# Kernel optimization log

Measured on AMD Instinct MI355X. Metric: run time of the kernel, lower is better.

Reference implementation:

```python
import jax, jax.numpy as jnp
import numpy as np

ALPHA, BETA, THRESH, T = 0.9, 0.8, 1.0, 10


def _heaviside(x):
    return (x > 0).astype(x.dtype)


def _conv(x, w, b, stride):
    y = jax.lax.conv_general_dilated(
        x, w, window_strides=(stride, stride), padding='VALID',
        dimension_numbers=('NCHW', 'OIHW', 'NCHW'))
    return jax.nn.relu(y + b[None, :, None, None])


def setup_inputs() -> dict:
    key = jax.random.key(0)
    ks = jax.random.split(key, 16)
    B = 128
    state = jax.random.uniform(ks[0], (B, 3, 224, 224), dtype=jnp.float32)
    history = jax.random.uniform(ks[1], (B, 90), dtype=jnp.float32)
    fc_in = 64 * 24 * 24 + 90  # 36954

    def w(k, shape, fan_in):
        return jax.random.normal(k, shape, dtype=jnp.float32) * (1.0 / np.sqrt(fan_in))

    return {
        'state': state, 'history': history,
        'cw1': w(ks[2], (32, 3, 8, 8), 3 * 8 * 8), 'cb1': jnp.zeros((32,), jnp.float32),
        'cw2': w(ks[3], (64, 32, 4, 4), 32 * 4 * 4), 'cb2': jnp.zeros((64,), jnp.float32),
        'cw3': w(ks[4], (64, 64, 3, 3), 64 * 3 * 3), 'cb3': jnp.zeros((64,), jnp.float32),
        'w1': w(ks[5], (128, fc_in), fc_in), 'b1': jnp.zeros((128,), jnp.float32),
        'w2': w(ks[6], (256, 128), 128), 'b2': jnp.zeros((256,), jnp.float32),
        'w3': w(ks[7], (9, 256), 256), 'b3': jnp.zeros((9,), jnp.float32),
    }


def reference(state, history, cw1, cb1, cw2, cb2, cw3, cb3, w1, b1, w2, b2, w3, b3):
    B = state.shape[0]
    f = _conv(state, cw1, cb1, 4)
    f = _conv(f, cw2, cb2, 2)
    f = _conv(f, cw3, cb3, 1)
    x = jnp.concatenate([f.reshape(B, -1), history], axis=1)  # (B, 36954)
    # encoding='constant' -> input (hence h1) is identical every timestep
    h1 = x @ w1.T + b1  # (B,128)

    def lif(h, mem, syn):
        new_syn = ALPHA * syn + h
        new_mem = BETA * mem + new_syn
        out = _heaviside(new_mem - THRESH)
        return out, new_mem - out * THRESH, new_syn

    z = lambda d: jnp.zeros((B, d), x.dtype)
    carry0 = (z(128), z(128), z(256), z(256), z(9), z(9), z(9))

    def step(carry, _):
        mem1, syn1, mem2, syn2, mem3, syn3, pot = carry
        spk1, mem1, syn1 = lif(h1, mem1, syn1)
        h2 = spk1 @ w2.T + b2
        spk2, mem2, syn2 = lif(h2, mem2, syn2)
        h3 = spk2 @ w3.T + b3
        syn3 = ALPHA * syn3 + h3
        mem3 = BETA * mem3 + syn3
        pot = pot + mem3
        return (mem1, syn1, mem2, syn2, mem3, syn3, pot), None

    carry, _ = jax.lax.scan(step, carry0, None, length=T)
    return carry[6] / T
```

## Files before the change

kernel.cpp:

```cpp
#include <hip/hip_runtime.h>

#define ALPHA 0.9f
#define BETA  0.8f
#define XS 36960

typedef _Float16 f16;
typedef _Float16 f16x8 __attribute__((ext_vector_type(8)));
typedef float f32x4 __attribute__((ext_vector_type(4)));


__global__ __launch_bounds__(256) void prep_weights_kernel(
    const float* __restrict__ cw1, const float* __restrict__ cw2,
    const float* __restrict__ cw3, const float* __restrict__ w2,
    f16* __restrict__ w1h, f16* __restrict__ w1l,
    f16* __restrict__ w2h, f16* __restrict__ w2l,
    f16* __restrict__ w3h, f16* __restrict__ w3l,
    float* __restrict__ w2q) {
  int i = blockIdx.x * 256 + threadIdx.x;
  if (i < 6144)  { float v = cw1[i]; f16 h = (f16)v; w1h[i] = h; w1l[i] = (f16)(v - (float)h); }
  if (i < 32768) { float v = cw2[i]; f16 h = (f16)v; w2h[i] = h; w2l[i] = (f16)(v - (float)h); }
  if (i < 49152) {
    int oc = i / 768, r = i % 768;
    int c = r / 12, rr = r % 12, kh = rr >> 2, kw = rr & 3;
    float v = (kw < 3) ? cw3[oc * 576 + c * 9 + kh * 3 + kw] : 0.f;
    f16 h = (f16)v; w3h[i] = h; w3l[i] = (f16)(v - (float)h);
  }
  if (i < 32768) {
    int j = i >> 7, k = i & 127;
    w2q[((k >> 2) * 256 + j) * 4 + (k & 3)] = w2[i];
  }
}

__global__ __launch_bounds__(256) void pad_w1_kernel(
    const float* __restrict__ w1, float* __restrict__ w1p) {
  int i = blockIdx.x * 256 + threadIdx.x;
  if (i < 128 * 18480) {
    int j = i / 18480, c = i - j * 18480;
    float2 v;
    if (c < 18477) v = *(const float2*)&w1[(size_t)j * 36954 + c * 2];
    else v = make_float2(0.f, 0.f);
    *(float2*)&w1p[(size_t)j * XS + c * 2] = v;
  }
}

__global__ __launch_bounds__(256) void conv1_direct_kernel(
    const float* __restrict__ in, const f16* __restrict__ wh,
    const f16* __restrict__ wl, const float* __restrict__ bias,
    float* __restrict__ out) {
  constexpr int K = 192, KCH = 6;
  constexpr int OW = 55, OHW = 3025;
  __shared__ f16 Ah[2 * KCH * 512], Al[2 * KCH * 512];

  const int n = blockIdx.y;
  const int pos0 = blockIdx.x * 128;
  const int t = threadIdx.x;
  const int w = t >> 6, lane = t & 63, quad = lane >> 4, l16 = lane & 15;
  const size_t in_n = (size_t)n * 3 * 224 * 224;

  for (int s = t; s < 2 * KCH * 64; s += 256) {
    int mt = s / (KCH * 64), rem = s % (KCH * 64);
    int kt = rem / 64, l = rem % 64;
    int oc = mt * 16 + (l & 15), kof = kt * 32 + (l >> 4) * 8;
    *(f16x8*)&Ah[s * 8] = *(const f16x8*)&wh[oc * K + kof];
    *(f16x8*)&Al[s * 8] = *(const f16x8*)&wl[oc * K + kof];
  }

  int ohS[2], owS[2], posv[2];
#pragma unroll
  for (int ntl = 0; ntl < 2; ++ntl) {
    int pos = pos0 + (w * 2 + ntl) * 16 + l16;
    posv[ntl] = pos;
    if (pos > OHW - 1) pos = OHW - 1;
    int oh = pos / OW, ow = pos - oh * OW;
    ohS[ntl] = oh * 4; owS[ntl] = ow * 4;
  }

  f32x4 acc[2][2] = {};
  __syncthreads();

#pragma unroll 2
  for (int kt = 0; kt < KCH; ++kt) {
    int r = kt * 4 + quad;
    int c = r >> 3, kh = r & 7;
    f16x8 bh[2], bl[2];
#pragma unroll
    for (int ntl = 0; ntl < 2; ++ntl) {
      const float* p = in + in_n +
          ((size_t)(c * 224 + ohS[ntl] + kh)) * 224 + owS[ntl];
      float4 v0 = *(const float4*)p;
      float4 v1 = *(const float4*)(p + 4);
      float vv[8] = {v0.x, v0.y, v0.z, v0.w, v1.x, v1.y, v1.z, v1.w};
#pragma unroll
      for (int e = 0; e < 8; ++e) {
        f16 h = (f16)vv[e];
        bh[ntl][e] = h;
        bl[ntl][e] = (f16)(vv[e] - (float)h);
      }
    }
    f16x8 ah0 = *(const f16x8*)&Ah[(0 * KCH + kt) * 512 + lane * 8];
    f16x8 ah1 = *(const f16x8*)&Ah[(1 * KCH + kt) * 512 + lane * 8];
    f16x8 al0 = *(const f16x8*)&Al[(0 * KCH + kt) * 512 + lane * 8];
    f16x8 al1 = *(const f16x8*)&Al[(1 * KCH + kt) * 512 + lane * 8];
    acc[0][0] = __builtin_amdgcn_mfma_f32_16x16x32_f16(ah0, bh[0], acc[0][0], 0, 0, 0);
    acc[0][0] = __builtin_amdgcn_mfma_f32_16x16x32_f16(ah0, bl[0], acc[0][0], 0, 0, 0);
    acc[0][0] = __builtin_amdgcn_mfma_f32_16x16x32_f16(al0, bh[0], acc[0][0], 0, 0, 0);
    acc[1][0] = __builtin_amdgcn_mfma_f32_16x16x32_f16(ah1, bh[0], acc[1][0], 0, 0, 0);
    acc[1][0] = __builtin_amdgcn_mfma_f32_16x16x32_f16(ah1, bl[0], acc[1][0], 0, 0, 0);
    acc[1][0] = __builtin_amdgcn_mfma_f32_16x16x32_f16(al1, bh[0], acc[1][0], 0, 0, 0);
    acc[0][1] = __builtin_amdgcn_mfma_f32_16x16x32_f16(ah0, bh[1], acc[0][1], 0, 0, 0);
    acc[0][1] = __builtin_amdgcn_mfma_f32_16x16x32_f16(ah0, bl[1], acc[0][1], 0, 0, 0);
    acc[0][1] = __builtin_amdgcn_mfma_f32_16x16x32_f16(al0, bh[1], acc[0][1], 0, 0, 0);
    acc[1][1] = __builtin_amdgcn_mfma_f32_16x16x32_f16(ah1, bh[1], acc[1][1], 0, 0, 0);
    acc[1][1] = __builtin_amdgcn_mfma_f32_16x16x32_f16(ah1, bl[1], acc[1][1], 0, 0, 0);
    acc[1][1] = __builtin_amdgcn_mfma_f32_16x16x32_f16(al1, bh[1], acc[1][1], 0, 0, 0);
  }

#pragma unroll
  for (int mtl = 0; mtl < 2; ++mtl)
#pragma unroll
    for (int ntl = 0; ntl < 2; ++ntl)
#pragma unroll
      for (int r = 0; r < 4; ++r) {
        int oc  = mtl * 16 + quad * 4 + r;
        int pos = posv[ntl];
        if (pos < OHW) {
          float v = acc[mtl][ntl][r] + bias[oc];
          v = v > 0.f ? v : 0.f;
          out[((size_t)n * 32 + oc) * OHW + pos] = v;
        }
      }
}

template<int IC, int KH, int KWP, int KWV, int S, int IH, int IW,
         int OW, int OHW, int OC, int NPB, bool OUT_X>
__global__ __launch_bounds__(256) void mfma_conv_kernel(
    const float* __restrict__ in, const f16* __restrict__ wh,
    const f16* __restrict__ wl, const float* __restrict__ bias,
    float* __restrict__ out) {
  constexpr int K = IC * KH * KWP;
  constexpr int KCH = K / 32;
  constexpr int MTILES = OC / 16;
  constexpr int NTILES = NPB / 16;
  constexpr int WOC = MTILES / 2;
  constexpr int ASLOTS = OC * 4;
  constexpr int BSLOTS = NPB * 4;
  constexpr int SITER = BSLOTS / 256;
  __shared__ f16 Ah[MTILES * 512], Al[MTILES * 512];
  __shared__ f16 Bh[NTILES * 512], Bl[NTILES * 512];

  const int n = blockIdx.y;
  const int pos0 = blockIdx.x * NPB;
  const int t = threadIdx.x;
  const int w = t >> 6, lane = t & 63, quad = lane >> 4, l16 = lane & 15;
  const int woc  = (WOC == 1) ? 0 : (w & 1);
  const int wpos = (WOC == 1) ? w : (w >> 1);
  const size_t in_n = (size_t)n * IC * IH * IW;

  int ohS[SITER], owS[SITER], kq8[SITER];
#pragma unroll
  for (int si = 0; si < SITER; ++si) {
    int s = t + si * 256;
    int nt = s >> 6, prem = s & 15;
    int pos = pos0 + nt * 16 + prem;
    if (pos > OHW - 1) pos = OHW - 1;
    int oh = pos / OW, ow = pos - oh * OW;
    ohS[si] = oh * S; owS[si] = ow * S;
    kq8[si] = ((s >> 4) & 3) * 8;
  }
  const int am = (t >> 6) * 16 + (t & 15);
  const int ak = ((t >> 4) & 3) * 8;

  f32x4 acc[2][2] = {};

  for (int kt = 0; kt < KCH; ++kt) {
    __syncthreads();
    if (t < ASLOTS) {
      *(f16x8*)&Ah[t * 8] = *(const f16x8*)&wh[am * K + kt * 32 + ak];
      *(f16x8*)&Al[t * 8] = *(const f16x8*)&wl[am * K + kt * 32 + ak];
    }
#pragma unroll
    for (int si = 0; si < SITER; ++si) {
      int s = t + si * 256;
      int kb = kt * 32 + kq8[si];
      f16x8 bh, bl;
#pragma unroll
      for (int half = 0; half < 2; ++half) {
        int kk = kb + half * 4;
        int kw0 = kk & (KWP - 1);
        int row = kk / KWP;
        int c = row / KH, kh = row - c * KH;
        const float* p = in + in_n +
            ((size_t)c * IH + ohS[si] + kh) * IW + owS[si] + kw0;
#pragma unroll
        for (int e = 0; e < 4; ++e) {
          float v = (KWV < KWP && e >= KWV) ? 0.f : p[e];
          f16 h = (f16)v;
          bh[half * 4 + e] = h;
          bl[half * 4 + e] = (f16)(v - (float)h);
        }
      }
      *(f16x8*)&Bh[s * 8] = bh;
      *(f16x8*)&Bl[s * 8] = bl;
    }
    __syncthreads();
    f16x8 ah0 = *(const f16x8*)&Ah[(woc * 2 + 0) * 512 + lane * 8];
    f16x8 ah1 = *(const f16x8*)&Ah[(woc * 2 + 1) * 512 + lane * 8];
    f16x8 al0 = *(const f16x8*)&Al[(woc * 2 + 0) * 512 + lane * 8];
    f16x8 al1 = *(const f16x8*)&Al[(woc * 2 + 1) * 512 + lane * 8];
    f16x8 bh0 = *(const f16x8*)&Bh[(wpos * 2 + 0) * 512 + lane * 8];
    f16x8 bh1 = *(const f16x8*)&Bh[(wpos * 2 + 1) * 512 + lane * 8];
    f16x8 bl0 = *(const f16x8*)&Bl[(wpos * 2 + 0) * 512 + lane * 8];
    f16x8 bl1 = *(const f16x8*)&Bl[(wpos * 2 + 1) * 512 + lane * 8];
    acc[0][0] = __builtin_amdgcn_mfma_f32_16x16x32_f16(ah0, bh0, acc[0][0], 0, 0, 0);
    acc[0][0] = __builtin_amdgcn_mfma_f32_16x16x32_f16(ah0, bl0, acc[0][0], 0, 0, 0);
    acc[0][0] = __builtin_amdgcn_mfma_f32_16x16x32_f16(al0, bh0, acc[0][0], 0, 0, 0);
    acc[1][0] = __builtin_amdgcn_mfma_f32_16x16x32_f16(ah1, bh0, acc[1][0], 0, 0, 0);
    acc[1][0] = __builtin_amdgcn_mfma_f32_16x16x32_f16(ah1, bl0, acc[1][0], 0, 0, 0);
    acc[1][0] = __builtin_amdgcn_mfma_f32_16x16x32_f16(al1, bh0, acc[1][0], 0, 0, 0);
    acc[0][1] = __builtin_amdgcn_mfma_f32_16x16x32_f16(ah0, bh1, acc[0][1], 0, 0, 0);
    acc[0][1] = __builtin_amdgcn_mfma_f32_16x16x32_f16(ah0, bl1, acc[0][1], 0, 0, 0);
    acc[0][1] = __builtin_amdgcn_mfma_f32_16x16x32_f16(al0, bh1, acc[0][1], 0, 0, 0);
    acc[1][1] = __builtin_amdgcn_mfma_f32_16x16x32_f16(ah1, bh1, acc[1][1], 0, 0, 0);
    acc[1][1] = __builtin_amdgcn_mfma_f32_16x16x32_f16(ah1, bl1, acc[1][1], 0, 0, 0);
    acc[1][1] = __builtin_amdgcn_mfma_f32_16x16x32_f16(al1, bh1, acc[1][1], 0, 0, 0);
  }
#pragma unroll
  for (int mtl = 0; mtl < 2; ++mtl)
#pragma unroll
    for (int ntl = 0; ntl < 2; ++ntl)
#pragma unroll
      for (int r = 0; r < 4; ++r) {
        int oc  = (woc * 2 + mtl) * 16 + quad * 4 + r;
        int pos = pos0 + (wpos * 2 + ntl) * 16 + l16;
        if (pos < OHW) {
          float v = acc[mtl][ntl][r] + bias[oc];
          v = v > 0.f ? v : 0.f;
          if (OUT_X)
            out[(size_t)n * XS + oc * OHW + pos] = v;
          else
            out[((size_t)n * OC + oc) * OHW + pos] = v;
        }
      }
}

__global__ __launch_bounds__(256) void histpack_kernel(
    const float* __restrict__ h, float* __restrict__ x) {
  int i = blockIdx.x * 256 + threadIdx.x;
  if (i < 128 * 96) {
    int n = i / 96, k = i % 96;
    x[(size_t)n * XS + 36864 + k] = (k < 90) ? h[n * 90 + k] : 0.f;
  }
}

#define FC1_KT 289
__global__ __launch_bounds__(256) void fc1_kernel(
    const float* __restrict__ x, const float* __restrict__ w1p,
    float* __restrict__ P) {
  int kt = blockIdx.x;
  int t  = threadIdx.x;
  int bq = t & 15, jq = t >> 4;
  __shared__ float xs[128 * 36];
  __shared__ float wsm[128 * 36];
  float acc[8][8];
#pragma unroll
  for (int bb = 0; bb < 8; ++bb)
#pragma unroll
    for (int jj = 0; jj < 8; ++jj) acc[bb][jj] = 0.f;

  int cs = t & 7;
  int rs = t >> 3;
#pragma unroll 1
  for (int s = 0; s < 4; ++s) {
    int k0 = kt * 128 + s * 32;
    __syncthreads();
#pragma unroll
    for (int p = 0; p < 4; ++p) {
      int r = rs + p * 32;
      int gk = k0 + cs * 4;
      float4 xv, wv;
      if (gk < 36954) {
        xv = *(const float4*)&x[(size_t)r * XS + gk];
        wv = *(const float4*)&w1p[(size_t)r * XS + gk];
      } else {
        xv = make_float4(0.f, 0.f, 0.f, 0.f);
        wv = make_float4(0.f, 0.f, 0.f, 0.f);
      }
      *(float4*)&xs[r * 36 + cs * 4] = xv;
      *(float4*)&wsm[r * 36 + cs * 4] = wv;
    }
    __syncthreads();
#pragma unroll 1
    for (int kk = 0; kk < 32; kk += 4) {
      float4 xv[8], wv[8];
#pragma unroll
      for (int i = 0; i < 8; ++i)
        xv[i] = *(const float4*)&xs[(bq + 16 * i) * 36 + kk];
#pragma unroll
      for (int i = 0; i < 8; ++i)
        wv[i] = *(const float4*)&wsm[(jq + 16 * i) * 36 + kk];
#pragma unroll
      for (int bb = 0; bb < 8; ++bb)
#pragma unroll
        for (int jj = 0; jj < 8; ++jj) {
          acc[bb][jj] = fmaf(xv[bb].x, wv[jj].x, acc[bb][jj]);
          acc[bb][jj] = fmaf(xv[bb].y, wv[jj].y, acc[bb][jj]);
          acc[bb][jj] = fmaf(xv[bb].z, wv[jj].z, acc[bb][jj]);
          acc[bb][jj] = fmaf(xv[bb].w, wv[jj].w, acc[bb][jj]);
        }
    }
  }
  float* Pb = P + (size_t)kt * 16384;
#pragma unroll
  for (int bb = 0; bb < 8; ++bb)
#pragma unroll
    for (int jj = 0; jj < 8; ++jj)
      Pb[(bq + 16 * bb) * 128 + jq + 16 * jj] = acc[bb][jj];
}

__global__ __launch_bounds__(256) void reduce_p_kernel(
    const float* __restrict__ P, const float* __restrict__ b1,
    float* __restrict__ h1s) {
  int idx = blockIdx.x * 256 + threadIdx.x;
  int j = idx & 127;
  float a0 = 0.f, a1 = 0.f, a2 = 0.f, a3 = 0.f;
  int kt = 0;
#pragma unroll 2
  for (; kt + 3 < FC1_KT; kt += 4) {
    a0 += P[(size_t)(kt + 0) * 16384 + idx];
    a1 += P[(size_t)(kt + 1) * 16384 + idx];
    a2 += P[(size_t)(kt + 2) * 16384 + idx];
    a3 += P[(size_t)(kt + 3) * 16384 + idx];
  }
  for (; kt < FC1_KT; ++kt) a0 += P[(size_t)kt * 16384 + idx];
  h1s[idx] = ((a0 + a1) + (a2 + a3)) + b1[j];
}

__global__ __launch_bounds__(256, 1) void recur_kernel(
    const float* __restrict__ h1s,
    const float4* __restrict__ w2q,
    const float* __restrict__ b2,
    const float* __restrict__ w3,
    const float* __restrict__ b3,
    float* __restrict__ out) {
  int b = blockIdx.x;
  int t = threadIdx.x;
  __shared__ float spk1s[128];
  __shared__ float spk2s[256];
  __shared__ float w3s[9 * 256];
  __shared__ float part[9][16];
  float4 w2c[32];
#pragma unroll
  for (int k4 = 0; k4 < 32; ++k4) w2c[k4] = w2q[k4 * 256 + t];
  for (int i = t; i < 9 * 256; i += 256) w3s[i] = w3[i];
  float h1 = (t < 128) ? h1s[b * 128 + t] : 0.f;
  float mem1 = 0.f, syn1 = 0.f, mem2 = 0.f, syn2 = 0.f;
  float b2v = b2[t];
  float mem3 = 0.f, syn3 = 0.f, pot = 0.f;
  float b3v = (t < 9) ? b3[t] : 0.f;
  int j3 = t >> 4, p = t & 15;
  __syncthreads();

  for (int step = 0; step < 10; ++step) {
    if (t < 128) {
      syn1 = ALPHA * syn1 + h1;
      mem1 = BETA * mem1 + syn1;
      float s = (mem1 > 1.0f) ? 1.0f : 0.0f;
      mem1 -= s;
      spk1s[t] = s;
    }
    __syncthreads();
    float h2 = b2v;
#pragma unroll
    for (int k4 = 0; k4 < 32; ++k4) {
      float4 s = *(const float4*)&spk1s[k4 * 4];
      h2 = fmaf(s.x, w2c[k4].x, h2);
      h2 = fmaf(s.y, w2c[k4].y, h2);
      h2 = fmaf(s.z, w2c[k4].z, h2);
      h2 = fmaf(s.w, w2c[k4].w, h2);
    }
    syn2 = ALPHA * syn2 + h2;
    mem2 = BETA * mem2 + syn2;
    float s2 = (mem2 > 1.0f) ? 1.0f : 0.0f;
    mem2 -= s2;
    spk2s[t] = s2;
    __syncthreads();
    if (t < 144) {
      float a = 0.f;
      const float* wr = &w3s[j3 * 256 + p * 16];
      const float* sp = &spk2s[p * 16];
#pragma unroll
      for (int e = 0; e < 16; ++e) a = fmaf(sp[e], wr[e], a);
      part[j3][p] = a;
    }
    __syncthreads();
    if (t < 9) {
      float a = b3v;
#pragma unroll
      for (int p2 = 0; p2 < 16; ++p2) a += part[t][p2];
      syn3 = ALPHA * syn3 + a;
      mem3 = BETA * mem3 + syn3;
      pot += mem3;
    }
  }
  if (t < 9) out[b * 9 + t] = pot * 0.1f;
}

extern "C" void kernel_launch(void* const* d_in, const int* in_sizes, int n_in,
                              void* d_out, int out_size, void* d_ws, size_t ws_size,
                              hipStream_t stream) {
  const float* state   = (const float*)d_in[0];
  const float* history = (const float*)d_in[1];
  const float* cw1 = (const float*)d_in[2];
  const float* cb1 = (const float*)d_in[3];
  const float* cw2 = (const float*)d_in[4];
  const float* cb2 = (const float*)d_in[5];
  const float* cw3 = (const float*)d_in[6];
  const float* cb3 = (const float*)d_in[7];
  const float* w1  = (const float*)d_in[8];
  const float* b1  = (const float*)d_in[9];
  const float* w2  = (const float*)d_in[10];
  const float* b2  = (const float*)d_in[11];
  const float* w3  = (const float*)d_in[12];
  const float* b3  = (const float*)d_in[13];
  float* out = (float*)d_out;
  char* ws = (char*)d_ws;

  float* f1  = (float*)(ws + 0);
  float* xb  = (float*)(ws + 0);
  float* w1p = (float*)(ws + 18923520);
  float* f2  = (float*)(ws + 49561600);
  float* P   = (float*)(ws + 49561600);
  f16* wf1h = (f16*)(ws + 71712768);
  f16* wf1l = (f16*)(ws + 71725056);
  f16* wf2h = (f16*)(ws + 71737344);
  f16* wf2l = (f16*)(ws + 71802880);
  f16* wf3h = (f16*)(ws + 71868416);
  f16* wf3l = (f16*)(ws + 71966720);
  float* w2q = (float*)(ws + 72065024);
  float* h1s = (float*)(ws + 72196096);

  prep_weights_kernel<<<192, 256, 0, stream>>>(cw1, cw2, cw3, w2,
                                               wf1h, wf1l, wf2h, wf2l,
                                               wf3h, wf3l, w2q);
  conv1_direct_kernel<<<dim3(24, 128), 256, 0, stream>>>(state, wf1h, wf1l, cb1, f1);
  mfma_conv_kernel<32, 4, 4, 4, 2, 55, 55, 26, 676, 64, 64, false>
      <<<dim3(11, 128), 256, 0, stream>>>(f1, wf2h, wf2l, cb2, f2);
  pad_w1_kernel<<<9240, 256, 0, stream>>>(w1, w1p);
  mfma_conv_kernel<64, 3, 4, 3, 1, 26, 26, 24, 576, 64, 64, true>
      <<<dim3(9, 128), 256, 0, stream>>>(f2, wf3h, wf3l, cb3, xb);
  histpack_kernel<<<48, 256, 0, stream>>>(history, xb);
  fc1_kernel<<<FC1_KT, 256, 0, stream>>>(xb, w1p, P);
  reduce_p_kernel<<<64, 256, 0, stream>>>(P, b1, h1s);
  recur_kernel<<<128, 256, 0, stream>>>(h1s, (const float4*)w2q, b2, w3, b3, out);
}
```

Before: 344.8 us.

## Store conv activations as packed hi/lo fp16 pairs and stage conv1 via LDS

Conv1 and conv2 now write their outputs as packed (high, low) fp16 pairs in one u32, so the following conv reads pre-split values and rebuilds the hi/lo f16x8 operands with byte permutes instead of converting from fp32 each time. Conv1 now loads its input patches into LDS with global_load_lds and loads weights per k-chunk instead of all up front. The generic conv kernel drops its separate Bh/Bl split stage and keeps one B buffer per half-row. Intermediate traffic stays at 4 bytes per element while the repeated float-to-split conversion in the im2col path goes away, at the cost of extra barriers and per-chunk weight loads in conv1.

Result: no change. 351.6 us (+2.0%).

```diff
diff --git a/kernel.cpp b/kernel.cpp
--- a/kernel.cpp
+++ b/kernel.cpp
@@ -7,6 +7,34 @@
 typedef _Float16 f16;
 typedef _Float16 f16x8 __attribute__((ext_vector_type(8)));
 typedef float f32x4 __attribute__((ext_vector_type(4)));
+typedef unsigned int u32;
+
+#define GLOAD_LDS16(gsrc, ldst)                                        \
+  __builtin_amdgcn_global_load_lds(                                    \
+      (const __attribute__((address_space(1))) void*)(gsrc),           \
+      (__attribute__((address_space(3))) void*)(ldst), 16, 0, 0)
+
+__device__ inline u32 hpair(u32 d0, u32 d1) {
+#if __has_builtin(__builtin_amdgcn_perm)
+  return __builtin_amdgcn_perm(d1, d0, 0x05040100u);
+#else
+  return (d0 & 0xffffu) | (d1 << 16);
+#endif
+}
+__device__ inline u32 lpair(u32 d0, u32 d1) {
+#if __has_builtin(__builtin_amdgcn_perm)
+  return __builtin_amdgcn_perm(d1, d0, 0x07060302u);
+#else
+  return (d0 >> 16) | (d1 & 0xffff0000u);
+#endif
+}
+
+__device__ inline u32 pack_hl(float v) {
+  f16 h = (f16)v;
+  f16 l = (f16)(v - (float)h);
+  return (u32)__builtin_bit_cast(unsigned short, h) |
+         ((u32)__builtin_bit_cast(unsigned short, l) << 16);
+}
 
 
 __global__ __launch_bounds__(256) void prep_weights_kernel(
@@ -43,52 +71,68 @@
   }
 }
 
-__global__ __launch_bounds__(256) void conv1_direct_kernel(
+__global__ __launch_bounds__(256) void conv1_kernel(
     const float* __restrict__ in, const f16* __restrict__ wh,
     const f16* __restrict__ wl, const float* __restrict__ bias,
-    float* __restrict__ out) {
-  constexpr int K = 192, KCH = 6;
-  constexpr int OW = 55, OHW = 3025;
-  __shared__ f16 Ah[2 * KCH * 512], Al[2 * KCH * 512];
-
-  const int n = blockIdx.y;
-  const int pos0 = blockIdx.x * 128;
+    u32* __restrict__ out) {
+  constexpr int K = 192, KCH = 6, OW = 55, OHW = 3025, NPB = 128;
+  __shared__ __attribute__((aligned(16))) f16 Ah[2 * 512], Al[2 * 512];
+  __shared__ __attribute__((aligned(16))) float Bf[8 * 512];
+
+  const int n = blockIdx.y, pos0 = blockIdx.x * NPB;
   const int t = threadIdx.x;
   const int w = t >> 6, lane = t & 63, quad = lane >> 4, l16 = lane & 15;
-  const size_t in_n = (size_t)n * 3 * 224 * 224;
-
-  for (int s = t; s < 2 * KCH * 64; s += 256) {
-    int mt = s / (KCH * 64), rem = s % (KCH * 64);
-    int kt = rem / 64, l = rem % 64;
-    int oc = mt * 16 + (l & 15), kof = kt * 32 + (l >> 4) * 8;
-    *(f16x8*)&Ah[s * 8] = *(const f16x8*)&wh[oc * K + kof];
-    *(f16x8*)&Al[s * 8] = *(const f16x8*)&wl[oc * K + kof];
-  }
-
-  int ohS[2], owS[2], posv[2];
-#pragma unroll
-  for (int ntl = 0; ntl < 2; ++ntl) {
-    int pos = pos0 + (w * 2 + ntl) * 16 + l16;
-    posv[ntl] = pos;
+  const float* __restrict__ inb = in + (size_t)n * 3 * 224 * 224;
+
+  const int rq = (t >> 4) & 3;
+  int base[2];
+#pragma unroll
+  for (int si = 0; si < 2; ++si) {
+    int s = t + si * 256;
+    int pos = pos0 + (s >> 6) * 16 + (s & 15);
     if (pos > OHW - 1) pos = OHW - 1;
     int oh = pos / OW, ow = pos - oh * OW;
-    ohS[ntl] = oh * 4; owS[ntl] = ow * 4;
-  }
+    base[si] = oh * 4 * 224 + ow * 4;
+  }
+  const int am = (t >> 6) * 16 + (t & 15);
+  const int ak = ((t >> 4) & 3) * 8;
+
+  int posv[2];
+#pragma unroll
+  for (int ntl = 0; ntl < 2; ++ntl)
+    posv[ntl] = pos0 + (w * 2 + ntl) * 16 + l16;
 
   f32x4 acc[2][2] = {};
-  __syncthreads();
-
-#pragma unroll 2
+
   for (int kt = 0; kt < KCH; ++kt) {
-    int r = kt * 4 + quad;
-    int c = r >> 3, kh = r & 7;
+    __syncthreads();
+    if (t < 128) {
+      *(f16x8*)&Ah[t * 8] = *(const f16x8*)&wh[am * K + kt * 32 + ak];
+      *(f16x8*)&Al[t * 8] = *(const f16x8*)&wl[am * K + kt * 32 + ak];
+    }
+    {
+      int r = kt * 4 + rq;
+      int c = r >> 3, kh = r & 7;
+      int rowoff = c * 50176 + kh * 224;
+#pragma unroll
+      for (int si = 0; si < 2; ++si)
+#pragma unroll
+        for (int half = 0; half < 2; ++half)
+          GLOAD_LDS16(inb + rowoff + base[si] + half * 4,
+                      &Bf[(si * 4 + w) * 512 + half * 256]);
+    }
+    __syncthreads();
+
+    f16x8 ah0 = *(const f16x8*)&Ah[0 * 512 + lane * 8];
+    f16x8 ah1 = *(const f16x8*)&Ah[1 * 512 + lane * 8];
+    f16x8 al0 = *(const f16x8*)&Al[0 * 512 + lane * 8];
+    f16x8 al1 = *(const f16x8*)&Al[1 * 512 + lane * 8];
     f16x8 bh[2], bl[2];
 #pragma unroll
     for (int ntl = 0; ntl < 2; ++ntl) {
-      const float* p = in + in_n +
-          ((size_t)(c * 224 + ohS[ntl] + kh)) * 224 + owS[ntl];
-      float4 v0 = *(const float4*)p;
-      float4 v1 = *(const float4*)(p + 4);
+      const float* bp = &Bf[(w * 2 + ntl) * 512 + lane * 4];
+      float4 v0 = *(const float4*)bp;
+      float4 v1 = *(const float4*)(bp + 256);
       float vv[8] = {v0.x, v0.y, v0.z, v0.w, v1.x, v1.y, v1.z, v1.w};
 #pragma unroll
       for (int e = 0; e < 8; ++e) {
@@ -97,10 +141,6 @@
         bl[ntl][e] = (f16)(vv[e] - (float)h);
       }
     }
-    f16x8 ah0 = *(const f16x8*)&Ah[(0 * KCH + kt) * 512 + lane * 8];
-    f16x8 ah1 = *(const f16x8*)&Ah[(1 * KCH + kt) * 512 + lane * 8];
-    f16x8 al0 = *(const f16x8*)&Al[(0 * KCH + kt) * 512 + lane * 8];
-    f16x8 al1 = *(const f16x8*)&Al[(1 * KCH + kt) * 512 + lane * 8];
     acc[0][0] = __builtin_amdgcn_mfma_f32_16x16x32_f16(ah0, bh[0], acc[0][0], 0, 0, 0);
     acc[0][0] = __builtin_amdgcn_mfma_f32_16x16x32_f16(ah0, bl[0], acc[0][0], 0, 0, 0);
     acc[0][0] = __builtin_amdgcn_mfma_f32_16x16x32_f16(al0, bh[0], acc[0][0], 0, 0, 0);
@@ -126,119 +166,106 @@
         if (pos < OHW) {
           float v = acc[mtl][ntl][r] + bias[oc];
           v = v > 0.f ? v : 0.f;
-          out[((size_t)n * 32 + oc) * OHW + pos] = v;
+          out[((size_t)n * 32 + oc) * OHW + pos] = pack_hl(v);
         }
       }
 }
 
 template<int IC, int KH, int KWP, int KWV, int S, int IH, int IW,
          int OW, int OHW, int OC, int NPB, bool OUT_X>
-__global__ __launch_bounds__(256) void mfma_conv_kernel(
-    const float* __restrict__ in, const f16* __restrict__ wh,
+__global__ __launch_bounds__(256) void convhl_kernel(
+    const u32* __restrict__ in, const f16* __restrict__ wh,
     const f16* __restrict__ wl, const float* __restrict__ bias,
-    float* __restrict__ out) {
+    void* __restrict__ outv) {
   constexpr int K = IC * KH * KWP;
   constexpr int KCH = K / 32;
-  constexpr int MTILES = OC / 16;
-  constexpr int NTILES = NPB / 16;
-  constexpr int WOC = MTILES / 2;
-  constexpr int ASLOTS = OC * 4;
-  constexpr int BSLOTS = NPB * 4;
-  constexpr int SITER = BSLOTS / 256;
-  __shared__ f16 Ah[MTILES * 512], Al[MTILES * 512];
-  __shared__ f16 Bh[NTILES * 512], Bl[NTILES * 512];
-
-  const int n = blockIdx.y;
-  const int pos0 = blockIdx.x * NPB;
+  __shared__ __attribute__((aligned(16))) f16 Ah[4 * 512], Al[4 * 512];
+  __shared__ __attribute__((aligned(16))) u32 Bhl[2][256 * 4];
+
+  const int n = blockIdx.y, pos0 = blockIdx.x * NPB;
   const int t = threadIdx.x;
   const int w = t >> 6, lane = t & 63, quad = lane >> 4, l16 = lane & 15;
-  const int woc  = (WOC == 1) ? 0 : (w & 1);
-  const int wpos = (WOC == 1) ? w : (w >> 1);
-  const size_t in_n = (size_t)n * IC * IH * IW;
-
-  int ohS[SITER], owS[SITER], kq8[SITER];
-#pragma unroll
-  for (int si = 0; si < SITER; ++si) {
-    int s = t + si * 256;
-    int nt = s >> 6, prem = s & 15;
-    int pos = pos0 + nt * 16 + prem;
-    if (pos > OHW - 1) pos = OHW - 1;
-    int oh = pos / OW, ow = pos - oh * OW;
-    ohS[si] = oh * S; owS[si] = ow * S;
-    kq8[si] = ((s >> 4) & 3) * 8;
-  }
+  const int woc = w & 1, wpos = w >> 1;
+  const u32* __restrict__ inb = in + (size_t)n * IC * IH * IW;
+
+  int pos = pos0 + (t >> 6) * 16 + (t & 15);
+  if (pos > OHW - 1) pos = OHW - 1;
+  int oh = pos / OW, ow = pos - oh * OW;
+  const int ohS = oh * S, owS = ow * S;
+  const int rq = ((t >> 4) & 3) * 2;
   const int am = (t >> 6) * 16 + (t & 15);
   const int ak = ((t >> 4) & 3) * 8;
 
+  int posv[2];
+#pragma unroll
+  for (int ntl = 0; ntl < 2; ++ntl)
+    posv[ntl] = pos0 + (wpos * 2 + ntl) * 16 + l16;
+
   f32x4 acc[2][2] = {};
 
   for (int kt = 0; kt < KCH; ++kt) {
     __syncthreads();
-    if (t < ASLOTS) {
-      *(f16x8*)&Ah[t * 8] = *(const f16x8*)&wh[am * K + kt * 32 + ak];
-      *(f16x8*)&Al[t * 8] = *(const f16x8*)&wl[am * K + kt * 32 + ak];
-    }
-#pragma unroll
-    for (int si = 0; si < SITER; ++si) {
-      int s = t + si * 256;
-      int kb = kt * 32 + kq8[si];
-      f16x8 bh, bl;
-#pragma unroll
-      for (int half = 0; half < 2; ++half) {
-        int kk = kb + half * 4;
-        int kw0 = kk & (KWP - 1);
-        int row = kk / KWP;
-        int c = row / KH, kh = row - c * KH;
-        const float* p = in + in_n +
-            ((size_t)c * IH + ohS[si] + kh) * IW + owS[si] + kw0;
-#pragma unroll
-        for (int e = 0; e < 4; ++e) {
-          float v = (KWV < KWP && e >= KWV) ? 0.f : p[e];
-          f16 h = (f16)v;
-          bh[half * 4 + e] = h;
-          bl[half * 4 + e] = (f16)(v - (float)h);
-        }
-      }
-      *(f16x8*)&Bh[s * 8] = bh;
-      *(f16x8*)&Bl[s * 8] = bl;
-    }
-    __syncthreads();
+    *(f16x8*)&Ah[t * 8] = *(const f16x8*)&wh[am * K + kt * 32 + ak];
+    *(f16x8*)&Al[t * 8] = *(const f16x8*)&wl[am * K + kt * 32 + ak];
+#pragma unroll
+    for (int half = 0; half < 2; ++half) {
+      int row = kt * 8 + rq + half;
+      int c = row / KH, kh = row - c * KH;
+      const u32* p = inb + ((size_t)c * IH + ohS + kh) * IW + owS;
+      uint4 d;
+      d.x = p[0]; d.y = p[1]; d.z = p[2];
+      d.w = (KWV < KWP) ? 0u : p[3];
+      *(uint4*)&Bhl[half][t * 4] = d;
+    }
+    __syncthreads();
+
     f16x8 ah0 = *(const f16x8*)&Ah[(woc * 2 + 0) * 512 + lane * 8];
     f16x8 ah1 = *(const f16x8*)&Ah[(woc * 2 + 1) * 512 + lane * 8];
     f16x8 al0 = *(const f16x8*)&Al[(woc * 2 + 0) * 512 + lane * 8];
     f16x8 al1 = *(const f16x8*)&Al[(woc * 2 + 1) * 512 + lane * 8];
-    f16x8 bh0 = *(const f16x8*)&Bh[(wpos * 2 + 0) * 512 + lane * 8];
-    f16x8 bh1 = *(const f16x8*)&Bh[(wpos * 2 + 1) * 512 + lane * 8];
-    f16x8 bl0 = *(const f16x8*)&Bl[(wpos * 2 + 0) * 512 + lane * 8];
-    f16x8 bl1 = *(const f16x8*)&Bl[(wpos * 2 + 1) * 512 + lane * 8];
-    acc[0][0] = __builtin_amdgcn_mfma_f32_16x16x32_f16(ah0, bh0, acc[0][0], 0, 0, 0);
-    acc[0][0] = __builtin_amdgcn_mfma_f32_16x16x32_f16(ah0, bl0, acc[0][0], 0, 0, 0);
-    acc[0][0] = __builtin_amdgcn_mfma_f32_16x16x32_f16(al0, bh0, acc[0][0], 0, 0, 0);
-    acc[1][0] = __builtin_amdgcn_mfma_f32_16x16x32_f16(ah1, bh0, acc[1][0], 0, 0, 0);
-    acc[1][0] = __builtin_amdgcn_mfma_f32_16x16x32_f16(ah1, bl0, acc[1][0], 0, 0, 0);
-    acc[1][0] = __builtin_amdgcn_mfma_f32_16x16x32_f16(al1, bh0, acc[1][0], 0, 0, 0);
-    acc[0][1] = __builtin_amdgcn_mfma_f32_16x16x32_f16(ah0, bh1, acc[0][1], 0, 0, 0);
-    acc[0][1] = __builtin_amdgcn_mfma_f32_16x16x32_f16(ah0, bl1, acc[0][1], 0, 0, 0);
-    acc[0][1] = __builtin_amdgcn_mfma_f32_16x16x32_f16(al0, bh1, acc[0][1], 0, 0, 0);
-    acc[1][1] = __builtin_amdgcn_mfma_f32_16x16x32_f16(ah1, bh1, acc[1][1], 0, 0, 0);
-    acc[1][1] = __builtin_amdgcn_mfma_f32_16x16x32_f16(ah1, bl1, acc[1][1], 0, 0, 0);
-    acc[1][1] = __builtin_amdgcn_mfma_f32_16x16x32_f16(al1, bh1, acc[1][1], 0, 0, 0);
-  }
+    f16x8 bh[2], bl[2];
+#pragma unroll
+    for (int ntl = 0; ntl < 2; ++ntl) {
+      int sl = ((wpos * 2 + ntl) * 64 + lane) * 4;
+      uint4 q0 = *(const uint4*)&Bhl[0][sl];
+      uint4 q1 = *(const uint4*)&Bhl[1][sl];
+      uint4 hv, lv;
+      hv.x = hpair(q0.x, q0.y); lv.x = lpair(q0.x, q0.y);
+      hv.y = hpair(q0.z, q0.w); lv.y = lpair(q0.z, q0.w);
+      hv.z = hpair(q1.x, q1.y); lv.z = lpair(q1.x, q1.y);
+      hv.w = hpair(q1.z, q1.w); lv.w = lpair(q1.z, q1.w);
+      bh[ntl] = __builtin_bit_cast(f16x8, hv);
+      bl[ntl] = __builtin_bit_cast(f16x8, lv);
+    }
+    acc[0][0] = __builtin_amdgcn_mfma_f32_16x16x32_f16(ah0, bh[0], acc[0][0], 0, 0, 0);
+    acc[0][0] = __builtin_amdgcn_mfma_f32_16x16x32_f16(ah0, bl[0], acc[0][0], 0, 0, 0);
+    acc[0][0] = __builtin_amdgcn_mfma_f32_16x16x32_f16(al0, bh[0], acc[0][0], 0, 0, 0);
+    acc[1][0] = __builtin_amdgcn_mfma_f32_16x16x32_f16(ah1, bh[0], acc[1][0], 0, 0, 0);
+    acc[1][0] = __builtin_amdgcn_mfma_f32_16x16x32_f16(ah1, bl[0], acc[1][0], 0, 0, 0);
+    acc[1][0] = __builtin_amdgcn_mfma_f32_16x16x32_f16(al1, bh[0], acc[1][0], 0, 0, 0);
+    acc[0][1] = __builtin_amdgcn_mfma_f32_16x16x32_f16(ah0, bh[1], acc[0][1], 0, 0, 0);
+    acc[0][1] = __builtin_amdgcn_mfma_f32_16x16x32_f16(ah0, bl[1], acc[0][1], 0, 0, 0);
+    acc[0][1] = __builtin_amdgcn_mfma_f32_16x16x32_f16(al0, bh[1], acc[0][1], 0, 0, 0);
+    acc[1][1] = __builtin_amdgcn_mfma_f32_16x16x32_f16(ah1, bh[1], acc[1][1], 0, 0, 0);
+    acc[1][1] = __builtin_amdgcn_mfma_f32_16x16x32_f16(ah1, bl[1], acc[1][1], 0, 0, 0);
+    acc[1][1] = __builtin_amdgcn_mfma_f32_16x16x32_f16(al1, bh[1], acc[1][1], 0, 0, 0);
+  }
+
 #pragma unroll
   for (int mtl = 0; mtl < 2; ++mtl)
 #pragma unroll
     for (int ntl = 0; ntl < 2; ++ntl)
 #pragma unroll
       for (int r = 0; r < 4; ++r) {
-        int oc  = (woc * 2 + mtl) * 16 + quad * 4 + r;
-        int pos = pos0 + (wpos * 2 + ntl) * 16 + l16;
-        if (pos < OHW) {
+        int oc = (woc * 2 + mtl) * 16 + quad * 4 + r;
+        int p2 = posv[ntl];
+        if (p2 < OHW) {
           float v = acc[mtl][ntl][r] + bias[oc];
           v = v > 0.f ? v : 0.f;
-          if (OUT_X)
-            out[(size_t)n * XS + oc * OHW + pos] = v;
+          if constexpr (OUT_X)
+            ((float*)outv)[(size_t)n * XS + oc * OHW + p2] = v;
           else
-            out[((size_t)n * OC + oc) * OHW + pos] = v;
+            ((u32*)outv)[((size_t)n * OC + oc) * OHW + p2] = pack_hl(v);
         }
       }
 }
@@ -425,11 +452,11 @@
   float* out = (float*)d_out;
   char* ws = (char*)d_ws;
 
-  float* f1  = (float*)(ws + 0);
-  float* xb  = (float*)(ws + 0);
-  float* w1p = (float*)(ws + 18923520);
-  float* f2  = (float*)(ws + 49561600);
-  float* P   = (float*)(ws + 49561600);
+  u32*   f1hl = (u32*)(ws + 0);
+  float* xb   = (float*)(ws + 0);
+  float* w1p  = (float*)(ws + 18923520);
+  u32*   f2hl = (u32*)(ws + 49561600);
+  float* P    = (float*)(ws + 49561600);
   f16* wf1h = (f16*)(ws + 71712768);
   f16* wf1l = (f16*)(ws + 71725056);
   f16* wf2h = (f16*)(ws + 71737344);
@@ -442,12 +469,12 @@
   prep_weights_kernel<<<192, 256, 0, stream>>>(cw1, cw2, cw3, w2,
                                                wf1h, wf1l, wf2h, wf2l,
                                                wf3h, wf3l, w2q);
-  conv1_direct_kernel<<<dim3(24, 128), 256, 0, stream>>>(state, wf1h, wf1l, cb1, f1);
-  mfma_conv_kernel<32, 4, 4, 4, 2, 55, 55, 26, 676, 64, 64, false>
-      <<<dim3(11, 128), 256, 0, stream>>>(f1, wf2h, wf2l, cb2, f2);
+  conv1_kernel<<<dim3(24, 128), 256, 0, stream>>>(state, wf1h, wf1l, cb1, f1hl);
+  convhl_kernel<32, 4, 4, 4, 2, 55, 55, 26, 676, 64, 64, false>
+      <<<dim3(11, 128), 256, 0, stream>>>(f1hl, wf2h, wf2l, cb2, (void*)f2hl);
   pad_w1_kernel<<<9240, 256, 0, stream>>>(w1, w1p);
-  mfma_conv_kernel<64, 3, 4, 3, 1, 26, 26, 24, 576, 64, 64, true>
-      <<<dim3(9, 128), 256, 0, stream>>>(f2, wf3h, wf3l, cb3, xb);
+  convhl_kernel<64, 3, 4, 3, 1, 26, 26, 24, 576, 64, 64, true>
+      <<<dim3(9, 128), 256, 0, stream>>>(f2hl, wf3h, wf3l, cb3, (void*)xb);
   histpack_kernel<<<48, 256, 0, stream>>>(history, xb);
   fc1_kernel<<<FC1_KT, 256, 0, stream>>>(xb, w1p, P);
   reduce_p_kernel<<<64, 256, 0, stream>>>(P, b1, h1s);
```
